# Kernel tuning notes

Measured on AMD Instinct MI355X. Metric: run time of the kernel, lower is better.

The kernel has to match this reference:

```python
import jax, jax.numpy as jnp
import numpy as np

H = 256      # hidden_units
NB = 2       # num_blocks
NH = 4       # num_heads
E = 8        # num_experts
K = 2        # top_k
L = 200      # maxlen
B = 128      # batch
ITEM = 100000
USER = 50000


def _ln(x, w, b, eps):
    m = x.mean(-1, keepdims=True)
    v = ((x - m) ** 2).mean(-1, keepdims=True)
    return (x - m) / jnp.sqrt(v + eps) * w + b


def setup_inputs() -> dict:
    key = jax.random.key(0)
    ks = iter(jax.random.split(key, 48))

    def n(shape, s=0.02):
        return jax.random.normal(next(ks), shape, jnp.float32) * s

    item_emb = n((ITEM + 1, H)).at[0].set(0.0)   # padding_idx=0
    pos_emb = n((L + 1, H)).at[0].set(0.0)
    user_emb = n((USER + 1, H)).at[0].set(0.0)
    return dict(
        user_ids=jax.random.randint(next(ks), (B,), 1, USER + 1),
        log_seqs=jax.random.randint(next(ks), (B, L), 0, ITEM + 1),
        item_ids=jax.random.randint(next(ks), (B,), 1, ITEM + 1),
        item_emb=item_emb, pos_emb=pos_emb, user_emb=user_emb,
        ln1_w=jnp.ones((NB, H)), ln1_b=jnp.zeros((NB, H)),
        inproj_w=n((NB, 3 * H, H)), inproj_b=jnp.zeros((NB, 3 * H)),
        outproj_w=n((NB, H, H)), outproj_b=jnp.zeros((NB, H)),
        ln2_w=jnp.ones((NB, H)), ln2_b=jnp.zeros((NB, H)),
        gate_w=n((NB, E, H)), gate_b=jnp.zeros((NB, E)),
        e_w1=n((NB, E, H, H)), e_b1=jnp.zeros((NB, E, H)),
        e_w2=n((NB, E, H, H)), e_b2=jnp.zeros((NB, E, H)),
        moeln_w=jnp.ones((NB, H)), moeln_b=jnp.zeros((NB, H)),
        lastln_w=jnp.ones((H,)), lastln_b=jnp.zeros((H,)),
    )


def reference(user_ids, log_seqs, item_ids, item_emb, pos_emb, user_emb,
              ln1_w, ln1_b, inproj_w, inproj_b, outproj_w, outproj_b,
              ln2_w, ln2_b, gate_w, gate_b, e_w1, e_b1, e_w2, e_b2,
              moeln_w, moeln_b, lastln_w, lastln_b):
    hd = H // NH
    # embeddings (padding id 0 -> zero rows)
    x = item_emb[log_seqs] * jnp.sqrt(jnp.float32(H))          # [B,L,H]
    poss = jnp.arange(1, L + 1)[None, :] * (log_seqs != 0)      # 0 where padded
    x = x + pos_emb[poss]
    causal = jnp.tril(jnp.ones((L, L), bool))

    for i in range(NB):
        # pre-LN query, raw x as key/value (matches original)
        q_in = _ln(x, ln1_w[i], ln1_b[i], 1e-8)
        wq, wk, wv = jnp.split(inproj_w[i], 3, axis=0)
        bq, bk, bv = jnp.split(inproj_b[i], 3)
        q = (q_in @ wq.T + bq).reshape(B, L, NH, hd)
        k = (x @ wk.T + bk).reshape(B, L, NH, hd)
        v = (x @ wv.T + bv).reshape(B, L, NH, hd)
        s = jnp.einsum('bqnd,bknd->bnqk', q, k) / jnp.sqrt(jnp.float32(hd))
        s = jnp.where(causal, s, -jnp.inf)
        a = jax.nn.softmax(s, axis=-1)
        ctx = jnp.einsum('bnqk,bknd->bqnd', a, v).reshape(B, L, H)
        mha = ctx @ outproj_w[i].T + outproj_b[i]
        x = q_in + mha
        x = _ln(x, ln2_w[i], ln2_b[i], 1e-8)

        # SparseMoE: top-k gate, all-expert dense compute, masked combine
        gl = jnp.einsum('bsh,eh->bse', x, gate_w[i]) + gate_b[i]
        w, idx = jax.lax.top_k(gl, K)
        w = jax.nn.softmax(w, axis=-1)
        comb = (jax.nn.one_hot(idx, E) * w[..., None]).sum(-2)   # [B,L,E]
        h = jax.nn.relu(jnp.einsum('bsh,ehd->besd', x, e_w1[i])
                        + e_b1[i][None, :, None, :])              # [B,E,L,H]
        y = jnp.einsum('besd,edh->besh', h, e_w2[i]) + e_b2[i][None, :, None, :]
        moe = jnp.einsum('bse,besh->bsh', comb, y)
        x = _ln(x + moe, moeln_w[i], moeln_b[i], 1e-5)

    x = _ln(x, lastln_w, lastln_b, 1e-8)
    final = x[:, -1, :] + user_emb[user_ids]
    return (final * item_emb[item_ids]).sum(-1)   # [B] logits
```

## Files before the change

kernel.cpp:

```cpp
#include <hip/hip_runtime.h>
#include <math.h>

#define H 256
#define NHEAD 4
#define HD 64
#define NEXP 8
#define SEQL 200
#define BATCH 128
#define NF (BATCH*SEQL)
#define KT 64
#define QT 64
#define QW 8

__device__ __forceinline__ float blk_sum256(float v, float* s4) {
    #pragma unroll
    for (int o = 32; o > 0; o >>= 1) v += __shfl_xor(v, o, 64);
    __syncthreads();
    if ((threadIdx.x & 63) == 0) s4[threadIdx.x >> 6] = v;
    __syncthreads();
    return s4[0] + s4[1] + s4[2] + s4[3];
}

__global__ __launch_bounds__(256) void embed_ln_kernel(
    const int* __restrict__ seqs, const float* __restrict__ item_emb,
    const float* __restrict__ pos_emb, float* __restrict__ x,
    float* __restrict__ xln, const float* __restrict__ w, const float* __restrict__ b)
{
    __shared__ float s4[4];
    int n = blockIdx.x, t = threadIdx.x;
    int id = seqs[n];
    int pos = (id != 0) ? (n % SEQL) + 1 : 0;
    float v = item_emb[(size_t)id*H + t] * 16.0f + pos_emb[(size_t)pos*H + t];
    x[(size_t)n*H + t] = v;
    float mean = blk_sum256(v, s4) * (1.f/H);
    float d = v - mean;
    float var = blk_sum256(d*d, s4) * (1.f/H);
    xln[(size_t)n*H + t] = d * rsqrtf(var + 1e-8f) * w[t] + b[t];
}

__global__ __launch_bounds__(256) void ln_kernel(
    const float* __restrict__ in, const float* __restrict__ res,
    float* __restrict__ out, const float* __restrict__ w, const float* __restrict__ b,
    float eps, int base, int step)
{
    __shared__ float s4[4];
    int r = blockIdx.x, t = threadIdx.x;
    float v = in[(size_t)(base + r*step)*H + t];
    if (res) v += res[(size_t)r*H + t];
    float mean = blk_sum256(v, s4) * (1.f/H);
    float d = v - mean;
    float var = blk_sum256(d*d, s4) * (1.f/H);
    out[(size_t)r*H + t] = d * rsqrtf(var + eps) * w[t] + b[t];
}

__global__ __launch_bounds__(256) void ln2_gate_kernel(
    const float* __restrict__ in, const float* __restrict__ res,
    float* __restrict__ out, const float* __restrict__ w, const float* __restrict__ b,
    const float* __restrict__ gw, const float* __restrict__ gb,
    int* __restrict__ top_idx, float* __restrict__ top_w)
{
    __shared__ float s4[4];
    __shared__ float xs[H];
    __shared__ float gl[NEXP];
    int n = blockIdx.x, t = threadIdx.x;
    float v = in[(size_t)n*H + t] + res[(size_t)n*H + t];
    float mean = blk_sum256(v, s4) * (1.f/H);
    float d = v - mean;
    float var = blk_sum256(d*d, s4) * (1.f/H);
    float r = d * rsqrtf(var + 1e-8f) * w[t] + b[t];
    out[(size_t)n*H + t] = r;
    xs[t] = r;
    __syncthreads();
    int wv = t >> 6, lane = t & 63;
    float xv[4];
    #pragma unroll
    for (int c = 0; c < 4; ++c) xv[c] = xs[lane + (c<<6)];
    #pragma unroll
    for (int s = 0; s < 2; ++s) {
        int e = wv*2 + s;
        float acc = 0.f;
        #pragma unroll
        for (int c = 0; c < 4; ++c) acc += xv[c] * gw[(size_t)e*H + lane + (c<<6)];
        #pragma unroll
        for (int o = 32; o > 0; o >>= 1) acc += __shfl_xor(acc, o, 64);
        if (lane == 0) gl[e] = acc + gb[e];
    }
    __syncthreads();
    if (t == 0) {
        int i0 = 0;
        for (int e = 1; e < NEXP; ++e) if (gl[e] > gl[i0]) i0 = e;
        int i1 = -1;
        for (int e = 0; e < NEXP; ++e) { if (e == i0) continue; if (i1 < 0 || gl[e] > gl[i1]) i1 = e; }
        float e1 = expf(gl[i1] - gl[i0]);
        float w0 = 1.f / (1.f + e1);
        top_idx[n*2+0] = i0; top_idx[n*2+1] = i1;
        top_w[n*2+0] = w0;  top_w[n*2+1] = 1.f - w0;
    }
}

__global__ __launch_bounds__(256) void moe_ln_kernel(
    const float* __restrict__ x, const float* __restrict__ ybuf,
    const int* __restrict__ tok_pair, const float* __restrict__ top_w,
    float* __restrict__ out, const float* __restrict__ w, const float* __restrict__ b,
    float eps)
{
    __shared__ float s4[4];
    int r = blockIdx.x, t = threadIdx.x;
    int p0 = tok_pair[r*2], p1 = tok_pair[r*2+1];
    float v = x[(size_t)r*H + t]
            + top_w[r*2+0] * ybuf[(size_t)p0*H + t]
            + top_w[r*2+1] * ybuf[(size_t)p1*H + t];
    float mean = blk_sum256(v, s4) * (1.f/H);
    float d = v - mean;
    float var = blk_sum256(d*d, s4) * (1.f/H);
    out[(size_t)r*H + t] = d * rsqrtf(var + eps) * w[t] + b[t];
}

__global__ __launch_bounds__(256) void gemm_nt(
    const float* __restrict__ A, const float* __restrict__ W,
    const float* __restrict__ bias, float* __restrict__ out, int nrows)
{
    __shared__ float As[16][68];
    __shared__ float Ws[16][68];
    int r0 = blockIdx.x * 64;
    if (r0 >= nrows) return;
    int c0 = blockIdx.y * 64;
    int tid = threadIdx.x;
    int tx = tid & 15, ty = tid >> 4;
    int lrow = tid >> 2, lkg = (tid & 3) << 2;
    float acc[4][4] = {};
    for (int kk = 0; kk < H; kk += 16) {
        float4 av = make_float4(0.f,0.f,0.f,0.f);
        int gr = r0 + lrow;
        if (gr < nrows) av = *(const float4*)(A + (size_t)gr*H + kk + lkg);
        As[lkg+0][lrow]=av.x; As[lkg+1][lrow]=av.y; As[lkg+2][lrow]=av.z; As[lkg+3][lrow]=av.w;
        float4 wv = *(const float4*)(W + (size_t)(c0+lrow)*H + kk + lkg);
        Ws[lkg+0][lrow]=wv.x; Ws[lkg+1][lrow]=wv.y; Ws[lkg+2][lrow]=wv.z; Ws[lkg+3][lrow]=wv.w;
        __syncthreads();
        #pragma unroll
        for (int k = 0; k < 16; ++k) {
            float4 a = *(const float4*)&As[k][ty<<2];
            float4 bv = *(const float4*)&Ws[k][tx<<2];
            float aa[4] = {a.x,a.y,a.z,a.w};
            float bb[4] = {bv.x,bv.y,bv.z,bv.w};
            #pragma unroll
            for (int ii = 0; ii < 4; ++ii)
                #pragma unroll
                for (int jj = 0; jj < 4; ++jj)
                    acc[ii][jj] += aa[ii] * bb[jj];
        }
        __syncthreads();
    }
    #pragma unroll
    for (int ii = 0; ii < 4; ++ii) {
        int gr = r0 + (ty<<2) + ii;
        if (gr < nrows) {
            #pragma unroll
            for (int jj = 0; jj < 4; ++jj) {
                int gc = c0 + (tx<<2) + jj;
                out[(size_t)gr*H + gc] = acc[ii][jj] + bias[gc];
            }
        }
    }
}

template<int GATHER, int RELU, int BT>
__device__ __forceinline__ void gemm128_body(
    const float* __restrict__ A, const float* __restrict__ W,
    const float* __restrict__ bias, float* __restrict__ out, int nrows,
    const int* __restrict__ pair_tok)
{
    __shared__ float As[2][16*132];
    __shared__ float Ws[2][16*132];
    int r0 = blockIdx.x * 128;
    if (r0 >= nrows) return;
    int c0 = blockIdx.y * 128;
    int tid = threadIdx.x;
    int tx = tid & 15, ty = tid >> 4;
    int lrow = tid >> 1, lkg = (tid & 1) << 3;
    int ar = r0 + lrow;
    bool va = ar < nrows;
    int ga = ar;
    if (GATHER) ga = va ? pair_tok[r0 + lrow] : 0;
    const float* ap = A + (size_t)(va ? ga : 0)*H + lkg;
    const float* wpT = W + (size_t)(c0 + lrow)*H + lkg;
    int kr0 = tid >> 5, cg = (tid & 31) << 2;
    const float* wpN0 = W + (size_t)kr0*H + c0 + cg;
    const float* wpN1 = wpN0 + (size_t)8*H;
    const float4 f4z = make_float4(0.f,0.f,0.f,0.f);
    float4 av0, av1, wv0, wv1;

#define G128_LOAD(S) {                                                        \
        int kk_ = (S)*16;                                                     \
        if (va) { av0 = *(const float4*)(ap + kk_);                           \
                  av1 = *(const float4*)(ap + kk_ + 4); }                     \
        else { av0 = f4z; av1 = f4z; }                                        \
        if (BT) { wv0 = *(const float4*)(wpT + kk_);                          \
                  wv1 = *(const float4*)(wpT + kk_ + 4); }                    \
        else { wv0 = *(const float4*)(wpN0 + (size_t)kk_*H);                  \
               wv1 = *(const float4*)(wpN1 + (size_t)kk_*H); } }

#define G128_WRITE(BI) {                                                      \
        float* as_ = As[BI]; float* ws_ = Ws[BI];                             \
        as_[(lkg+0)*132 + lrow]=av0.x; as_[(lkg+1)*132 + lrow]=av0.y;         \
        as_[(lkg+2)*132 + lrow]=av0.z; as_[(lkg+3)*132 + lrow]=av0.w;         \
        as_[(lkg+4)*132 + lrow]=av1.x; as_[(lkg+5)*132 + lrow]=av1.y;         \
        as_[(lkg+6)*132 + lrow]=av1.z; as_[(lkg+7)*132 + lrow]=av1.w;         \
        if (BT) {                                                             \
            ws_[(lkg+0)*132 + lrow]=wv0.x; ws_[(lkg+1)*132 + lrow]=wv0.y;     \
            ws_[(lkg+2)*132 + lrow]=wv0.z; ws_[(lkg+3)*132 + lrow]=wv0.w;     \
            ws_[(lkg+4)*132 + lrow]=wv1.x; ws_[(lkg+5)*132 + lrow]=wv1.y;     \
            ws_[(lkg+6)*132 + lrow]=wv1.z; ws_[(lkg+7)*132 + lrow]=wv1.w;     \
        } else {                                                              \
            *(float4*)&ws_[kr0*132 + cg]     = wv0;                           \
            *(float4*)&ws_[(kr0+8)*132 + cg] = wv1;                           \
        } }

    const int NS = H/16;
    float acc[8][8] = {};
    G128_LOAD(0)
    G128_WRITE(0)
    G128_LOAD(1)
    __syncthreads();
    for (int s = 0; s < NS; ++s) {
        int cur = s & 1;
        if (s + 1 < NS) {
            G128_WRITE((s+1) & 1)
            if (s + 2 < NS) G128_LOAD(s+2)
        }
        const float* as = As[cur];
        const float* bs = Ws[cur];
        #pragma unroll
        for (int k = 0; k < 16; ++k) {
            float4 a0 = *(const float4*)&as[k*132 + (ty<<2)];
            float4 a1 = *(const float4*)&as[k*132 + 64 + (ty<<2)];
            float4 b0 = *(const float4*)&bs[k*132 + (tx<<2)];
            float4 b1 = *(const float4*)&bs[k*132 + 64 + (tx<<2)];
            float aa[8] = {a0.x,a0.y,a0.z,a0.w,a1.x,a1.y,a1.z,a1.w};
            float bb[8] = {b0.x,b0.y,b0.z,b0.w,b1.x,b1.y,b1.z,b1.w};
            #pragma unroll
            for (int ii = 0; ii < 8; ++ii)
                #pragma unroll
                for (int jj = 0; jj < 8; ++jj)
                    acc[ii][jj] += aa[ii] * bb[jj];
        }
        __syncthreads();
    }
#undef G128_LOAD
#undef G128_WRITE
    #pragma unroll
    for (int hr = 0; hr < 2; ++hr)
        #pragma unroll
        for (int ii = 0; ii < 4; ++ii) {
            int row = r0 + 64*hr + (ty<<2) + ii;
            if (row < nrows) {
                #pragma unroll
                for (int hc = 0; hc < 2; ++hc) {
                    int col = c0 + 64*hc + (tx<<2);
                    #pragma unroll
                    for (int jj = 0; jj < 4; ++jj) {
                        float o = acc[4*hr+ii][4*hc+jj] + bias[col+jj];
                        if (RELU) o = fmaxf(o, 0.f);
                        out[(size_t)row*H + col + jj] = o;
                    }
                }
            }
        }
}

__global__ __launch_bounds__(256) void gemm_nt128z(
    const float* __restrict__ A0, const float* __restrict__ A1,
    const float* __restrict__ Wbase, const float* __restrict__ biasbase,
    float* __restrict__ outbase, int nrows)
{
    int z = blockIdx.z;
    const float* A = (z == 0) ? A0 : A1;
    gemm128_body<0,0,1>(A, Wbase + (size_t)z*H*H, biasbase + (size_t)z*H,
                        outbase + (size_t)z*NF*H, nrows, nullptr);
}

__global__ __launch_bounds__(256) void gemm_nt128(
    const float* __restrict__ A, const float* __restrict__ W,
    const float* __restrict__ bias, float* __restrict__ out, int nrows)
{
    gemm128_body<0,0,1>(A, W, bias, out, nrows, nullptr);
}

__global__ __launch_bounds__(256) void moe1_128(
    const float* __restrict__ X, const float* __restrict__ W1base,
    const float* __restrict__ b1base, const int* __restrict__ pair_tok,
    const int* __restrict__ offsets, const int* __restrict__ counts,
    float* __restrict__ hbuf)
{
    int e = blockIdx.z;
    int cnt = counts[e], off = offsets[e];
    gemm128_body<1,1,0>(X, W1base + (size_t)e*H*H, b1base + (size_t)e*H,
                        hbuf + (size_t)off*H, cnt, pair_tok + off);
}

__global__ __launch_bounds__(256) void moe2_128(
    const float* __restrict__ Hbuf, const float* __restrict__ W2base,
    const float* __restrict__ b2base, const int* __restrict__ offsets,
    const int* __restrict__ counts, float* __restrict__ ybuf)
{
    int e = blockIdx.z;
    int cnt = counts[e], off = offsets[e];
    gemm128_body<0,0,0>(Hbuf + (size_t)off*H, W2base + (size_t)e*H*H, b2base + (size_t)e*H,
                        ybuf + (size_t)off*H, cnt, nullptr);
}

__global__ __launch_bounds__(512) void attn_kernel(
    const float* __restrict__ qbuf, const float* __restrict__ kbuf,
    const float* __restrict__ vbuf, float* __restrict__ ctx, int nq, int nz)
{
    __shared__ float kv[KT*(HD+4)];
    __shared__ float qs[QT][HD+4];
    __shared__ float ps[QT][KT+4];
    int bx = blockIdx.x;
    int b = bx / nz, z = bx % nz;
    int h = blockIdx.y;
    int qbase = z * QT;
    int nqt = nq - qbase;
    if (nqt <= 0) return;
    if (nqt > QT) nqt = QT;
    int tid = threadIdx.x, w = tid >> 6, lane = tid & 63;
    int off = SEQL - nq;
    for (int i = tid; i < QT*(HD/4); i += 512) {
        int row = i >> 4, c4 = (i & 15) << 2;
        float4 qv = make_float4(0.f,0.f,0.f,0.f);
        if (row < nqt) qv = *(const float4*)(qbuf + (size_t)(b*nq + qbase + row)*H + h*HD + c4);
        *(float4*)&qs[row][c4] = qv;
    }
    float m[QW], l[QW], acc[QW];
    #pragma unroll
    for (int i = 0; i < QW; ++i) { m[i] = -3e30f; l[i] = 0.f; acc[i] = 0.f; }
    int wq0 = w * QW;
    int wqn = nqt - wq0; if (wqn > QW) wqn = QW;
    int wmaxpos = qbase + wq0 + (wqn > 0 ? wqn - 1 : 0) + off;
    int ntiles = (qbase + nqt - 1 + off) / KT + 1;
    int q_sub = lane >> 3, kq = lane & 7;
    for (int t = 0; t < ntiles; ++t) {
        int kbase = t * KT;
        bool active = (wqn > 0) && (kbase <= wmaxpos);
        __syncthreads();
        for (int i = tid; i < KT*(HD/4); i += 512) {
            int row = i >> 4, c4 = (i & 15) << 2;
            int key = kbase + row;
            float4 kvv = make_float4(0.f,0.f,0.f,0.f);
            if (key < SEQL) kvv = *(const float4*)(kbuf + (size_t)(b*SEQL + key)*H + h*HD + c4);
            *(float4*)&kv[row*(HD+4) + c4] = kvv;
        }
        __syncthreads();
        if (active) {
            float s[QW];
            #pragma unroll
            for (int qi = 0; qi < QW; ++qi) s[qi] = 0.f;
            #pragma unroll 4
            for (int d4 = 0; d4 < HD; d4 += 4) {
                float4 k4 = *(const float4*)&kv[lane*(HD+4) + d4];
                #pragma unroll
                for (int qi = 0; qi < QW; ++qi) {
                    float4 q4 = *(const float4*)&qs[wq0+qi][d4];
                    s[qi] += k4.x*q4.x + k4.y*q4.y + k4.z*q4.z + k4.w*q4.w;
                }
            }
            #pragma unroll
            for (int qi = 0; qi < QW; ++qi) {
                if (qi < wqn) {
                    int qpos = qbase + wq0 + qi + off;
                    bool valid = (kbase + lane) <= qpos;
                    ps[wq0+qi][lane] = valid ? s[qi]*0.125f : -3e30f;
                }
            }
        }
        __syncthreads();
        {
            int key = kbase + lane;
            bool kval = key < SEQL;
            const float* vp = vbuf + (size_t)(b*SEQL + (kval ? key : 0))*H + h*HD;
            #pragma unroll
            for (int it = 0; it < 2; ++it) {
                int c4 = ((it << 3) + w) << 2;
                float4 vv = make_float4(0.f,0.f,0.f,0.f);
                if (kval) vv = *(const float4*)(vp + c4);
                kv[(c4+0)*(KT+4) + lane] = vv.x;
                kv[(c4+1)*(KT+4) + lane] = vv.y;
                kv[(c4+2)*(KT+4) + lane] = vv.z;
                kv[(c4+3)*(KT+4) + lane] = vv.w;
            }
        }
        __syncthreads();
        if (active) {
            float mq = m[0];
            #pragma unroll
            for (int i = 1; i < QW; ++i) if (q_sub == i) mq = m[i];
            const float2* pr = (const float2*)&ps[wq0+q_sub][kq*8];
            float2 a0 = pr[0], a1 = pr[1], a2 = pr[2], a3 = pr[3];
            float mloc = fmaxf(fmaxf(fmaxf(a0.x,a0.y), fmaxf(a1.x,a1.y)),
                               fmaxf(fmaxf(a2.x,a2.y), fmaxf(a3.x,a3.y)));
            float tm = mloc;
            #pragma unroll
            for (int o = 1; o < 8; o <<= 1) tm = fmaxf(tm, __shfl_xor(tm, o, 64));
            float mn = fmaxf(mq, tm);
            float p0 = expf(a0.x-mn), p1 = expf(a0.y-mn), p2 = expf(a1.x-mn), p3 = expf(a1.y-mn);
            float p4 = expf(a2.x-mn), p5 = expf(a2.y-mn), p6 = expf(a3.x-mn), p7 = expf(a3.y-mn);
            float psum = ((p0+p1)+(p2+p3)) + ((p4+p5)+(p6+p7));
            #pragma unroll
            for (int o = 1; o < 8; o <<= 1) psum += __shfl_xor(psum, o, 64);
            float2* pw = (float2*)&ps[wq0+q_sub][kq*8];
            pw[0] = make_float2(p0,p1); pw[1] = make_float2(p2,p3);
            pw[2] = make_float2(p4,p5); pw[3] = make_float2(p6,p7);
            #pragma unroll
            for (int qi = 0; qi < QW; ++qi) {
                float tmv = __shfl(tm, qi*8, 64);
                float psv = __shfl(psum, qi*8, 64);
                if (qi < wqn) {
                    float mn2 = fmaxf(m[qi], tmv);
                    float scl = expf(m[qi] - mn2);
                    l[qi] = l[qi]*scl + psv;
                    acc[qi] *= scl;
                    m[qi] = mn2;
                }
            }
            #pragma unroll 4
            for (int k4 = 0; k4 < KT; k4 += 4) {
                float4 v4 = *(const float4*)&kv[lane*(KT+4) + k4];
                #pragma unroll
                for (int qi = 0; qi < QW; ++qi) {
                    if (qi < wqn) {
                        float4 p4v = *(const float4*)&ps[wq0+qi][k4];
                        acc[qi] += p4v.x*v4.x + p4v.y*v4.y + p4v.z*v4.z + p4v.w*v4.w;
                    }
                }
            }
        }
    }
    #pragma unroll
    for (int qi = 0; qi < QW; ++qi) {
        if (qi < wqn) {
            ctx[(size_t)(b*nq + qbase + wq0 + qi)*H + h*HD + lane] = acc[qi] / l[qi];
        }
    }
}

__global__ __launch_bounds__(256) void count_kernel(
    const int* __restrict__ top_idx, int* __restrict__ counts, int nrows)
{
    __shared__ int hist[NEXP];
    int tid = threadIdx.x;
    if (tid < NEXP) hist[tid] = 0;
    __syncthreads();
    int n = blockIdx.x * 256 + tid;
    if (n < nrows) {
        atomicAdd(&hist[top_idx[n*2+0]], 1);
        atomicAdd(&hist[top_idx[n*2+1]], 1);
    }
    __syncthreads();
    if (tid < NEXP && hist[tid] > 0) atomicAdd(&counts[tid], hist[tid]);
}

__global__ void scan_kernel(const int* __restrict__ counts, int* __restrict__ offsets,
                            int* __restrict__ cursor)
{
    int s = 0;
    for (int e = 0; e < NEXP; ++e) { offsets[e] = s; cursor[e] = s; s += counts[e]; }
}

__global__ __launch_bounds__(256) void scatter_kernel(
    const int* __restrict__ top_idx,
    int* __restrict__ cursor, int* __restrict__ pair_tok, int* __restrict__ tok_pair, int nrows)
{
    __shared__ int lcnt[NEXP];
    __shared__ int lbase[NEXP];
    int tid = threadIdx.x;
    if (tid < NEXP) lcnt[tid] = 0;
    __syncthreads();
    int n = blockIdx.x * 256 + tid;
    int e0 = 0, e1 = 0, p0 = 0, p1 = 0;
    bool act = n < nrows;
    if (act) {
        e0 = top_idx[n*2+0]; e1 = top_idx[n*2+1];
        p0 = atomicAdd(&lcnt[e0], 1);
        p1 = atomicAdd(&lcnt[e1], 1);
    }
    __syncthreads();
    if (tid < NEXP) lbase[tid] = (lcnt[tid] > 0) ? atomicAdd(&cursor[tid], lcnt[tid]) : 0;
    __syncthreads();
    if (act) {
        int q0 = lbase[e0] + p0, q1 = lbase[e1] + p1;
        pair_tok[q0] = n; pair_tok[q1] = n;
        tok_pair[n*2+0] = q0; tok_pair[n*2+1] = q1;
    }
}

__global__ __launch_bounds__(256) void moe_gemm1(
    const float* __restrict__ X, const float* __restrict__ W1base,
    const float* __restrict__ b1base, const int* __restrict__ pair_tok,
    const int* __restrict__ offsets, const int* __restrict__ counts,
    float* __restrict__ hbuf)
{
    int e = blockIdx.z;
    int cnt = counts[e];
    int r0 = blockIdx.x * 64;
    if (r0 >= cnt) return;
    int off = offsets[e];
    int c0 = blockIdx.y * 64;
    const float* W = W1base + (size_t)e * H * H;
    const float* bias = b1base + (size_t)e * H;
    __shared__ float As[16][68];
    __shared__ float Bs[16][68];
    int tid = threadIdx.x, tx = tid & 15, ty = tid >> 4;
    int lrow = tid >> 2, lkg = (tid & 3) << 2;
    float acc[4][4] = {};
    for (int kk = 0; kk < H; kk += 16) {
        float4 av = make_float4(0.f,0.f,0.f,0.f);
        int pr = r0 + lrow;
        if (pr < cnt) {
            int tok = pair_tok[off + pr];
            av = *(const float4*)(X + (size_t)tok*H + kk + lkg);
        }
        As[lkg+0][lrow]=av.x; As[lkg+1][lrow]=av.y; As[lkg+2][lrow]=av.z; As[lkg+3][lrow]=av.w;
        float4 wv = *(const float4*)(W + (size_t)(kk+ty)*H + c0 + (tx<<2));
        *(float4*)&Bs[ty][tx<<2] = wv;
        __syncthreads();
        #pragma unroll
        for (int k = 0; k < 16; ++k) {
            float4 a = *(const float4*)&As[k][ty<<2];
            float4 bv = *(const float4*)&Bs[k][tx<<2];
            float aa[4] = {a.x,a.y,a.z,a.w};
            float bb[4] = {bv.x,bv.y,bv.z,bv.w};
            #pragma unroll
            for (int ii = 0; ii < 4; ++ii)
                #pragma unroll
                for (int jj = 0; jj < 4; ++jj)
                    acc[ii][jj] += aa[ii] * bb[jj];
        }
        __syncthreads();
    }
    #pragma unroll
    for (int ii = 0; ii < 4; ++ii) {
        int pr = r0 + (ty<<2) + ii;
        if (pr < cnt) {
            #pragma unroll
            for (int jj = 0; jj < 4; ++jj) {
                int gc = c0 + (tx<<2) + jj;
                hbuf[(size_t)(off+pr)*H + gc] = fmaxf(acc[ii][jj] + bias[gc], 0.f);
            }
        }
    }
}

__global__ __launch_bounds__(256) void moe_gemm2(
    const float* __restrict__ Hbuf, const float* __restrict__ W2base,
    const float* __restrict__ b2base, const int* __restrict__ offsets,
    const int* __restrict__ counts, float* __restrict__ ybuf)
{
    int e = blockIdx.z;
    int cnt = counts[e];
    int r0 = blockIdx.x * 64;
    if (r0 >= cnt) return;
    int off = offsets[e];
    int c0 = blockIdx.y * 64;
    const float* W = W2base + (size_t)e * H * H;
    const float* bias = b2base + (size_t)e * H;
    __shared__ float As[16][68];
    __shared__ float Bs[16][68];
    int tid = threadIdx.x, tx = tid & 15, ty = tid >> 4;
    int lrow = tid >> 2, lkg = (tid & 3) << 2;
    float acc[4][4] = {};
    for (int kk = 0; kk < H; kk += 16) {
        float4 av = make_float4(0.f,0.f,0.f,0.f);
        int pr = r0 + lrow;
        if (pr < cnt) av = *(const float4*)(Hbuf + (size_t)(off+pr)*H + kk + lkg);
        As[lkg+0][lrow]=av.x; As[lkg+1][lrow]=av.y; As[lkg+2][lrow]=av.z; As[lkg+3][lrow]=av.w;
        float4 wv = *(const float4*)(W + (size_t)(kk+ty)*H + c0 + (tx<<2));
        *(float4*)&Bs[ty][tx<<2] = wv;
        __syncthreads();
        #pragma unroll
        for (int k = 0; k < 16; ++k) {
            float4 a = *(const float4*)&As[k][ty<<2];
            float4 bv = *(const float4*)&Bs[k][tx<<2];
            float aa[4] = {a.x,a.y,a.z,a.w};
            float bb[4] = {bv.x,bv.y,bv.z,bv.w};
            #pragma unroll
            for (int ii = 0; ii < 4; ++ii)
                #pragma unroll
                for (int jj = 0; jj < 4; ++jj)
                    acc[ii][jj] += aa[ii] * bb[jj];
        }
        __syncthreads();
    }
    #pragma unroll
    for (int ii = 0; ii < 4; ++ii) {
        int pr = r0 + (ty<<2) + ii;
        if (pr < cnt) {
            #pragma unroll
            for (int jj = 0; jj < 4; ++jj) {
                int gc = c0 + (tx<<2) + jj;
                ybuf[(size_t)(off+pr)*H + gc] = acc[ii][jj] + bias[gc];
            }
        }
    }
}

__global__ void zero_kernel(float* __restrict__ p, int n) {
    int i = blockIdx.x * 256 + threadIdx.x;
    if (i < n) p[i] = 0.f;
}

__global__ __launch_bounds__(256) void final_kernel(
    const float* __restrict__ xf, const float* __restrict__ lnw, const float* __restrict__ lnb,
    const float* __restrict__ user_emb, const float* __restrict__ item_emb,
    const int* __restrict__ user_ids, const int* __restrict__ item_ids, float* __restrict__ out)
{
    __shared__ float s4[4];
    int bb = blockIdx.x, t = threadIdx.x;
    float v = xf[(size_t)bb*H + t];
    float mean = blk_sum256(v, s4) * (1.f/H);
    float d = v - mean;
    float var = blk_sum256(d*d, s4) * (1.f/H);
    float lnv = d * rsqrtf(var + 1e-8f) * lnw[t] + lnb[t];
    float fin = lnv + user_emb[(size_t)user_ids[bb]*H + t];
    float prod = fin * item_emb[(size_t)item_ids[bb]*H + t];
    float tot = blk_sum256(prod, s4);
    if (t == 0) out[bb] = tot;
}

extern "C" void kernel_launch(void* const* d_in, const int* in_sizes, int n_in,
                              void* d_out, int out_size, void* d_ws, size_t ws_size,
                              hipStream_t stream)
{
    (void)in_sizes; (void)n_in; (void)out_size; (void)ws_size;
    const int*   user_ids  = (const int*)d_in[0];
    const int*   log_seqs  = (const int*)d_in[1];
    const int*   item_ids  = (const int*)d_in[2];
    const float* item_emb  = (const float*)d_in[3];
    const float* pos_emb   = (const float*)d_in[4];
    const float* user_emb  = (const float*)d_in[5];
    const float* ln1_w     = (const float*)d_in[6];
    const float* ln1_b     = (const float*)d_in[7];
    const float* inproj_w  = (const float*)d_in[8];
    const float* inproj_b  = (const float*)d_in[9];
    const float* outproj_w = (const float*)d_in[10];
    const float* outproj_b = (const float*)d_in[11];
    const float* ln2_w     = (const float*)d_in[12];
    const float* ln2_b     = (const float*)d_in[13];
    const float* gate_w    = (const float*)d_in[14];
    const float* gate_b    = (const float*)d_in[15];
    const float* e_w1      = (const float*)d_in[16];
    const float* e_b1      = (const float*)d_in[17];
    const float* e_w2      = (const float*)d_in[18];
    const float* e_b2      = (const float*)d_in[19];
    const float* moeln_w   = (const float*)d_in[20];
    const float* moeln_b   = (const float*)d_in[21];
    const float* lastln_w  = (const float*)d_in[22];
    const float* lastln_b  = (const float*)d_in[23];

    float* ws = (float*)d_ws;
    const size_t NFH = (size_t)NF * H;
    float* buf0 = ws;
    float* buf1 = buf0 + NFH;
    float* buf2 = buf1 + NFH;
    float* buf3 = buf2 + NFH;
    float* buf4 = buf3 + NFH;
    float* s0   = buf4 + NFH;
    float* s1   = s0 + (size_t)BATCH*H;
    float* s2   = s1 + (size_t)BATCH*H;
    float* s3   = s2 + (size_t)BATCH*H;
    float* s6   = s3 + (size_t)BATCH*H;
    float* s4   = s6 + (size_t)BATCH*H;
    float* s5   = s4 + (size_t)2*BATCH*H;
    float* top_w   = s5 + (size_t)2*BATCH*H;
    int*   top_idx = (int*)(top_w + (size_t)NF*2);
    int*   pair_tok= top_idx + (size_t)NF*2;
    int*   tok_pair= pair_tok + (size_t)NF*2;
    int*   counts  = tok_pair + (size_t)NF*2;
    int*   offsets = counts + NEXP;
    int*   cursor  = offsets + NEXP;

    dim3 blk(256);
    dim3 ablk(512);
    dim3 g128((NF+127)/128, H/128);
    dim3 g128z3((NF+127)/128, H/128, 3);
    dim3 g128z2((NF+127)/128, H/128, 2);
    dim3 gsmall((BATCH+63)/64, H/64);
    dim3 m128((NF+127)/128, H/128, NEXP);
    dim3 msmall((BATCH+63)/64, H/64, NEXP);

    {
        const int i = 0;
        const float* Wq = inproj_w + (size_t)i*3*H*H;
        const float* bq = inproj_b + (size_t)i*3*H;
        embed_ln_kernel<<<NF, blk, 0, stream>>>(log_seqs, item_emb, pos_emb, buf0, buf1,
                                                ln1_w + i*H, ln1_b + i*H);
        gemm_nt128z<<<g128z3, blk, 0, stream>>>(buf1, buf0, Wq, bq, buf2, NF);
        attn_kernel<<<dim3(BATCH*4, NHEAD), ablk, 0, stream>>>(buf2, buf3, buf4, buf2, SEQL, 4);
        gemm_nt128<<<g128, blk, 0, stream>>>(buf2, outproj_w + (size_t)i*H*H, outproj_b + i*H, buf3, NF);
        ln2_gate_kernel<<<NF, blk, 0, stream>>>(buf1, buf3, buf0, ln2_w + i*H, ln2_b + i*H,
                                                gate_w + (size_t)i*NEXP*H, gate_b + i*NEXP,
                                                top_idx, top_w);
        zero_kernel<<<1, 32, 0, stream>>>((float*)counts, NEXP);
        count_kernel<<<(NF+255)/256, blk, 0, stream>>>(top_idx, counts, NF);
        scan_kernel<<<1, 1, 0, stream>>>(counts, offsets, cursor);
        scatter_kernel<<<(NF+255)/256, blk, 0, stream>>>(top_idx, cursor, pair_tok, tok_pair, NF);
        moe1_128<<<m128, blk, 0, stream>>>(buf0, e_w1 + (size_t)i*NEXP*H*H, e_b1 + (size_t)i*NEXP*H,
                                           pair_tok, offsets, counts, buf3);
        moe2_128<<<m128, blk, 0, stream>>>(buf3, e_w2 + (size_t)i*NEXP*H*H, e_b2 + (size_t)i*NEXP*H,
                                           offsets, counts, buf1);
        moe_ln_kernel<<<NF, blk, 0, stream>>>(buf0, buf1, tok_pair, top_w, buf3,
                                              moeln_w + i*H, moeln_b + i*H, 1e-5f);
    }

    {
        const int i = 1;
        const float* Wq = inproj_w + (size_t)i*3*H*H;
        const float* bq = inproj_b + (size_t)i*3*H;
        float* X = buf3;
        ln_kernel<<<BATCH, blk, 0, stream>>>(X, nullptr, s0, ln1_w + i*H, ln1_b + i*H, 1e-8f, SEQL-1, SEQL);
        gemm_nt<<<gsmall, blk, 0, stream>>>(s0, Wq, bq, s1, BATCH);
        gemm_nt128z<<<g128z2, blk, 0, stream>>>(X, X, Wq + (size_t)H*H, bq + H, buf0, NF);
        attn_kernel<<<dim3(BATCH, NHEAD), ablk, 0, stream>>>(s1, buf0, buf1, s2, 1, 1);
        gemm_nt<<<gsmall, blk, 0, stream>>>(s2, outproj_w + (size_t)i*H*H, outproj_b + i*H, s3, BATCH);
        ln2_gate_kernel<<<BATCH, blk, 0, stream>>>(s0, s3, s2, ln2_w + i*H, ln2_b + i*H,
                                                   gate_w + (size_t)i*NEXP*H, gate_b + i*NEXP,
                                                   top_idx, top_w);
        zero_kernel<<<1, 32, 0, stream>>>((float*)counts, NEXP);
        count_kernel<<<1, blk, 0, stream>>>(top_idx, counts, BATCH);
        scan_kernel<<<1, 1, 0, stream>>>(counts, offsets, cursor);
        scatter_kernel<<<1, blk, 0, stream>>>(top_idx, cursor, pair_tok, tok_pair, BATCH);
        moe_gemm1<<<msmall, blk, 0, stream>>>(s2, e_w1 + (size_t)i*NEXP*H*H, e_b1 + (size_t)i*NEXP*H,
                                              pair_tok, offsets, counts, s4);
        moe_gemm2<<<msmall, blk, 0, stream>>>(s4, e_w2 + (size_t)i*NEXP*H*H, e_b2 + (size_t)i*NEXP*H,
                                              offsets, counts, s5);
        moe_ln_kernel<<<BATCH, blk, 0, stream>>>(s2, s5, tok_pair, top_w, s6,
                                                 moeln_w + i*H, moeln_b + i*H, 1e-5f);
    }

    final_kernel<<<BATCH, blk, 0, stream>>>(s6, lastln_w, lastln_b, user_emb, item_emb,
                                            user_ids, item_ids, (float*)d_out);
}
```

Measured before the change: 945.6 us.

## Replace FP32 SIMT GEMMs with split-bf16 MFMA GEMMs using pre-split weights

The large dense and MoE expert GEMMs change from FP32 register-tiled FMA loops to bf16 MFMA 16x16x32 instructions. Each operand is split into high and low bf16 parts and combined with three MFMAs, which keeps close to FP32 accuracy. Weights are split, and for the experts transposed, into bf16 hi/lo buffers by new kernels at the start of every call. Activations are split on the fly from global memory with no LDS staging, so A tiles are re-read once per column block. The attention grid is also reindexed to use blockIdx.z for query tiles.

```diff
diff --git a/kernel.cpp b/kernel.cpp
--- a/kernel.cpp
+++ b/kernel.cpp
@@ -12,6 +12,31 @@
 #define QT 64
 #define QW 8
 
+typedef __bf16 bf16x8 __attribute__((ext_vector_type(8)));
+typedef float  f32x4  __attribute__((ext_vector_type(4)));
+
+__device__ __forceinline__ void split8(const float* __restrict__ p, bf16x8& hi, bf16x8& lo, bool valid) {
+    if (valid) {
+        float4 a = *(const float4*)p;
+        float4 b = *(const float4*)(p + 4);
+        float x[8] = {a.x,a.y,a.z,a.w,b.x,b.y,b.z,b.w};
+        #pragma unroll
+        for (int j = 0; j < 8; ++j) {
+            __bf16 h = (__bf16)x[j];
+            hi[j] = h;
+            lo[j] = (__bf16)(x[j] - (float)h);
+        }
+    } else {
+        #pragma unroll
+        for (int j = 0; j < 8; ++j) { hi[j] = (__bf16)0.f; lo[j] = (__bf16)0.f; }
+    }
+}
+
+#define MFMA3(AH,AL,BH,BL,ACC) \
+    ACC = __builtin_amdgcn_mfma_f32_16x16x32_bf16(AH, BH, ACC, 0, 0, 0); \
+    ACC = __builtin_amdgcn_mfma_f32_16x16x32_bf16(AH, BL, ACC, 0, 0, 0); \
+    ACC = __builtin_amdgcn_mfma_f32_16x16x32_bf16(AL, BH, ACC, 0, 0, 0);
+
 __device__ __forceinline__ float blk_sum256(float v, float* s4) {
     #pragma unroll
     for (int o = 32; o > 0; o >>= 1) v += __shfl_xor(v, o, 64);
@@ -19,6 +44,31 @@
     if ((threadIdx.x & 63) == 0) s4[threadIdx.x >> 6] = v;
     __syncthreads();
     return s4[0] + s4[1] + s4[2] + s4[3];
+}
+
+__global__ __launch_bounds__(256) void split_plain(
+    const float* __restrict__ in, __bf16* __restrict__ hi, __bf16* __restrict__ lo, int n)
+{
+    for (int i = blockIdx.x * 256 + threadIdx.x; i < n; i += gridDim.x * 256) {
+        float x = in[i];
+        __bf16 h = (__bf16)x;
+        hi[i] = h;
+        lo[i] = (__bf16)(x - (float)h);
+    }
+}
+
+__global__ __launch_bounds__(256) void split_trans(
+    const float* __restrict__ in, __bf16* __restrict__ hi, __bf16* __restrict__ lo, int nmats)
+{
+    int n = nmats * H * H;
+    for (int i = blockIdx.x * 256 + threadIdx.x; i < n; i += gridDim.x * 256) {
+        int m = i / (H*H), rem = i % (H*H);
+        int nn = rem / H, k = rem % H;
+        float x = in[(size_t)m*H*H + (size_t)k*H + nn];
+        __bf16 h = (__bf16)x;
+        hi[i] = h;
+        lo[i] = (__bf16)(x - (float)h);
+    }
 }
 
 __global__ __launch_bounds__(256) void embed_ln_kernel(
@@ -164,161 +214,101 @@
     }
 }
 
-template<int GATHER, int RELU, int BT>
-__device__ __forceinline__ void gemm128_body(
-    const float* __restrict__ A, const float* __restrict__ W,
+template<int GATHER, int RELU>
+__device__ __forceinline__ void mfma64_body(
+    const float* __restrict__ A, const __bf16* __restrict__ Whi, const __bf16* __restrict__ Wlo,
     const float* __restrict__ bias, float* __restrict__ out, int nrows,
     const int* __restrict__ pair_tok)
 {
-    __shared__ float As[2][16*132];
-    __shared__ float Ws[2][16*132];
-    int r0 = blockIdx.x * 128;
+    int r0 = blockIdx.x * 64;
     if (r0 >= nrows) return;
-    int c0 = blockIdx.y * 128;
+    int c0 = blockIdx.y * 64;
     int tid = threadIdx.x;
-    int tx = tid & 15, ty = tid >> 4;
-    int lrow = tid >> 1, lkg = (tid & 1) << 3;
-    int ar = r0 + lrow;
-    bool va = ar < nrows;
-    int ga = ar;
-    if (GATHER) ga = va ? pair_tok[r0 + lrow] : 0;
-    const float* ap = A + (size_t)(va ? ga : 0)*H + lkg;
-    const float* wpT = W + (size_t)(c0 + lrow)*H + lkg;
-    int kr0 = tid >> 5, cg = (tid & 31) << 2;
-    const float* wpN0 = W + (size_t)kr0*H + c0 + cg;
-    const float* wpN1 = wpN0 + (size_t)8*H;
-    const float4 f4z = make_float4(0.f,0.f,0.f,0.f);
-    float4 av0, av1, wv0, wv1;
-
-#define G128_LOAD(S) {                                                        \
-        int kk_ = (S)*16;                                                     \
-        if (va) { av0 = *(const float4*)(ap + kk_);                           \
-                  av1 = *(const float4*)(ap + kk_ + 4); }                     \
-        else { av0 = f4z; av1 = f4z; }                                        \
-        if (BT) { wv0 = *(const float4*)(wpT + kk_);                          \
-                  wv1 = *(const float4*)(wpT + kk_ + 4); }                    \
-        else { wv0 = *(const float4*)(wpN0 + (size_t)kk_*H);                  \
-               wv1 = *(const float4*)(wpN1 + (size_t)kk_*H); } }
-
-#define G128_WRITE(BI) {                                                      \
-        float* as_ = As[BI]; float* ws_ = Ws[BI];                             \
-        as_[(lkg+0)*132 + lrow]=av0.x; as_[(lkg+1)*132 + lrow]=av0.y;         \
-        as_[(lkg+2)*132 + lrow]=av0.z; as_[(lkg+3)*132 + lrow]=av0.w;         \
-        as_[(lkg+4)*132 + lrow]=av1.x; as_[(lkg+5)*132 + lrow]=av1.y;         \
-        as_[(lkg+6)*132 + lrow]=av1.z; as_[(lkg+7)*132 + lrow]=av1.w;         \
-        if (BT) {                                                             \
-            ws_[(lkg+0)*132 + lrow]=wv0.x; ws_[(lkg+1)*132 + lrow]=wv0.y;     \
-            ws_[(lkg+2)*132 + lrow]=wv0.z; ws_[(lkg+3)*132 + lrow]=wv0.w;     \
-            ws_[(lkg+4)*132 + lrow]=wv1.x; ws_[(lkg+5)*132 + lrow]=wv1.y;     \
-            ws_[(lkg+6)*132 + lrow]=wv1.z; ws_[(lkg+7)*132 + lrow]=wv1.w;     \
-        } else {                                                              \
-            *(float4*)&ws_[kr0*132 + cg]     = wv0;                           \
-            *(float4*)&ws_[(kr0+8)*132 + cg] = wv1;                           \
-        } }
-
-    const int NS = H/16;
-    float acc[8][8] = {};
-    G128_LOAD(0)
-    G128_WRITE(0)
-    G128_LOAD(1)
-    __syncthreads();
-    for (int s = 0; s < NS; ++s) {
-        int cur = s & 1;
-        if (s + 1 < NS) {
-            G128_WRITE((s+1) & 1)
-            if (s + 2 < NS) G128_LOAD(s+2)
-        }
-        const float* as = As[cur];
-        const float* bs = Ws[cur];
+    int wid = tid >> 6, lane = tid & 63;
+    int wm = wid >> 1, wn = wid & 1;
+    int rbase = r0 + wm*32, cbase = c0 + wn*32;
+    int lr = lane & 15, lk = (lane >> 4) << 3;
+    f32x4 acc[2][2] = {};
+    int ar0 = rbase + lr, ar1 = ar0 + 16;
+    bool v0 = ar0 < nrows, v1 = ar1 < nrows;
+    int ga0 = ar0, ga1 = ar1;
+    if (GATHER) { ga0 = v0 ? pair_tok[ar0] : 0; ga1 = v1 ? pair_tok[ar1] : 0; }
+    const float* ap0 = A + (size_t)(v0 ? ga0 : 0)*H + lk;
+    const float* ap1 = A + (size_t)(v1 ? ga1 : 0)*H + lk;
+    size_t woff = (size_t)(cbase + lr)*H + lk;
+    #pragma unroll
+    for (int kk = 0; kk < H; kk += 32) {
+        bf16x8 ah0, al0, ah1, al1;
+        split8(ap0 + kk, ah0, al0, v0);
+        split8(ap1 + kk, ah1, al1, v1);
+        bf16x8 bh0 = *(const bf16x8*)(Whi + woff + kk);
+        bf16x8 bl0 = *(const bf16x8*)(Wlo + woff + kk);
+        bf16x8 bh1 = *(const bf16x8*)(Whi + woff + (size_t)16*H + kk);
+        bf16x8 bl1 = *(const bf16x8*)(Wlo + woff + (size_t)16*H + kk);
+        MFMA3(ah0, al0, bh0, bl0, acc[0][0]);
+        MFMA3(ah0, al0, bh1, bl1, acc[0][1]);
+        MFMA3(ah1, al1, bh0, bl0, acc[1][0]);
+        MFMA3(ah1, al1, bh1, bl1, acc[1][1]);
+    }
+    int lro = (lane >> 4) << 2;
+    #pragma unroll
+    for (int mi = 0; mi < 2; ++mi)
         #pragma unroll
-        for (int k = 0; k < 16; ++k) {
-            float4 a0 = *(const float4*)&as[k*132 + (ty<<2)];
-            float4 a1 = *(const float4*)&as[k*132 + 64 + (ty<<2)];
-            float4 b0 = *(const float4*)&bs[k*132 + (tx<<2)];
-            float4 b1 = *(const float4*)&bs[k*132 + 64 + (tx<<2)];
-            float aa[8] = {a0.x,a0.y,a0.z,a0.w,a1.x,a1.y,a1.z,a1.w};
-            float bb[8] = {b0.x,b0.y,b0.z,b0.w,b1.x,b1.y,b1.z,b1.w};
-            #pragma unroll
-            for (int ii = 0; ii < 8; ++ii)
-                #pragma unroll
-                for (int jj = 0; jj < 8; ++jj)
-                    acc[ii][jj] += aa[ii] * bb[jj];
-        }
-        __syncthreads();
-    }
-#undef G128_LOAD
-#undef G128_WRITE
-    #pragma unroll
-    for (int hr = 0; hr < 2; ++hr)
-        #pragma unroll
-        for (int ii = 0; ii < 4; ++ii) {
-            int row = r0 + 64*hr + (ty<<2) + ii;
-            if (row < nrows) {
-                #pragma unroll
-                for (int hc = 0; hc < 2; ++hc) {
-                    int col = c0 + 64*hc + (tx<<2);
-                    #pragma unroll
-                    for (int jj = 0; jj < 4; ++jj) {
-                        float o = acc[4*hr+ii][4*hc+jj] + bias[col+jj];
-                        if (RELU) o = fmaxf(o, 0.f);
-                        out[(size_t)row*H + col + jj] = o;
-                    }
+        for (int ni = 0; ni < 2; ++ni)
+            #pragma unroll
+            for (int j = 0; j < 4; ++j) {
+                int row = rbase + mi*16 + lro + j;
+                int col = cbase + ni*16 + lr;
+                if (row < nrows) {
+                    float o = acc[mi][ni][j] + bias[col];
+                    if (RELU) o = fmaxf(o, 0.f);
+                    out[(size_t)row*H + col] = o;
                 }
             }
-        }
-}
-
-__global__ __launch_bounds__(256) void gemm_nt128z(
+}
+
+__global__ __launch_bounds__(256) void mfma_z(
     const float* __restrict__ A0, const float* __restrict__ A1,
-    const float* __restrict__ Wbase, const float* __restrict__ biasbase,
-    float* __restrict__ outbase, int nrows)
+    const __bf16* __restrict__ Whi, const __bf16* __restrict__ Wlo,
+    const float* __restrict__ biasbase, float* __restrict__ outbase, int nrows)
 {
     int z = blockIdx.z;
     const float* A = (z == 0) ? A0 : A1;
-    gemm128_body<0,0,1>(A, Wbase + (size_t)z*H*H, biasbase + (size_t)z*H,
-                        outbase + (size_t)z*NF*H, nrows, nullptr);
-}
-
-__global__ __launch_bounds__(256) void gemm_nt128(
-    const float* __restrict__ A, const float* __restrict__ W,
-    const float* __restrict__ bias, float* __restrict__ out, int nrows)
-{
-    gemm128_body<0,0,1>(A, W, bias, out, nrows, nullptr);
-}
-
-__global__ __launch_bounds__(256) void moe1_128(
-    const float* __restrict__ X, const float* __restrict__ W1base,
+    mfma64_body<0,0>(A, Whi + (size_t)z*H*H, Wlo + (size_t)z*H*H,
+                     biasbase + (size_t)z*H, outbase + (size_t)z*NF*H, nrows, nullptr);
+}
+
+__global__ __launch_bounds__(256) void mfma_moe1(
+    const float* __restrict__ X, const __bf16* __restrict__ Whi, const __bf16* __restrict__ Wlo,
     const float* __restrict__ b1base, const int* __restrict__ pair_tok,
     const int* __restrict__ offsets, const int* __restrict__ counts,
     float* __restrict__ hbuf)
 {
     int e = blockIdx.z;
     int cnt = counts[e], off = offsets[e];
-    gemm128_body<1,1,0>(X, W1base + (size_t)e*H*H, b1base + (size_t)e*H,
-                        hbuf + (size_t)off*H, cnt, pair_tok + off);
-}
-
-__global__ __launch_bounds__(256) void moe2_128(
-    const float* __restrict__ Hbuf, const float* __restrict__ W2base,
+    mfma64_body<1,1>(X, Whi + (size_t)e*H*H, Wlo + (size_t)e*H*H,
+                     b1base + (size_t)e*H, hbuf + (size_t)off*H, cnt, pair_tok + off);
+}
+
+__global__ __launch_bounds__(256) void mfma_moe2(
+    const float* __restrict__ Hbuf, const __bf16* __restrict__ Whi, const __bf16* __restrict__ Wlo,
     const float* __restrict__ b2base, const int* __restrict__ offsets,
     const int* __restrict__ counts, float* __restrict__ ybuf)
 {
     int e = blockIdx.z;
     int cnt = counts[e], off = offsets[e];
-    gemm128_body<0,0,0>(Hbuf + (size_t)off*H, W2base + (size_t)e*H*H, b2base + (size_t)e*H,
-                        ybuf + (size_t)off*H, cnt, nullptr);
+    mfma64_body<0,0>(Hbuf + (size_t)off*H, Whi + (size_t)e*H*H, Wlo + (size_t)e*H*H,
+                     b2base + (size_t)e*H, ybuf + (size_t)off*H, cnt, nullptr);
 }
 
 __global__ __launch_bounds__(512) void attn_kernel(
     const float* __restrict__ qbuf, const float* __restrict__ kbuf,
-    const float* __restrict__ vbuf, float* __restrict__ ctx, int nq, int nz)
+    const float* __restrict__ vbuf, float* __restrict__ ctx, int nq)
 {
     __shared__ float kv[KT*(HD+4)];
     __shared__ float qs[QT][HD+4];
     __shared__ float ps[QT][KT+4];
-    int bx = blockIdx.x;
-    int b = bx / nz, z = bx % nz;
-    int h = blockIdx.y;
+    int b = blockIdx.x, h = blockIdx.y, z = blockIdx.z;
     int qbase = z * QT;
     int nqt = nq - qbase;
     if (nqt <= 0) return;
@@ -677,25 +667,40 @@
     int*   counts  = tok_pair + (size_t)NF*2;
     int*   offsets = counts + NEXP;
     int*   cursor  = offsets + NEXP;
+    const size_t W_IP = (size_t)2*3*H*H;
+    const size_t W_OP = (size_t)2*H*H;
+    const size_t W_E  = (size_t)2*NEXP*H*H;
+    __bf16* ip_hi = (__bf16*)(cursor + 64);
+    __bf16* ip_lo = ip_hi + W_IP;
+    __bf16* op_hi = ip_lo + W_IP;
+    __bf16* op_lo = op_hi + W_OP;
+    __bf16* e1_hi = op_lo + W_OP;
+    __bf16* e1_lo = e1_hi + W_E;
+    __bf16* e2_hi = e1_lo + W_E;
+    __bf16* e2_lo = e2_hi + W_E;
 
     dim3 blk(256);
     dim3 ablk(512);
-    dim3 g128((NF+127)/128, H/128);
-    dim3 g128z3((NF+127)/128, H/128, 3);
-    dim3 g128z2((NF+127)/128, H/128, 2);
+    dim3 m64z3(NF/64, H/64, 3);
+    dim3 m64z2(NF/64, H/64, 2);
+    dim3 m64z1(NF/64, H/64, 1);
+    dim3 m64e(NF/64, H/64, NEXP);
     dim3 gsmall((BATCH+63)/64, H/64);
-    dim3 m128((NF+127)/128, H/128, NEXP);
     dim3 msmall((BATCH+63)/64, H/64, NEXP);
+
+    split_plain<<<512, blk, 0, stream>>>(inproj_w,  ip_hi, ip_lo, (int)W_IP);
+    split_plain<<<256, blk, 0, stream>>>(outproj_w, op_hi, op_lo, (int)W_OP);
+    split_trans<<<1024, blk, 0, stream>>>(e_w1, e1_hi, e1_lo, 2*NEXP);
+    split_trans<<<1024, blk, 0, stream>>>(e_w2, e2_hi, e2_lo, 2*NEXP);
 
     {
         const int i = 0;
-        const float* Wq = inproj_w + (size_t)i*3*H*H;
         const float* bq = inproj_b + (size_t)i*3*H;
         embed_ln_kernel<<<NF, blk, 0, stream>>>(log_seqs, item_emb, pos_emb, buf0, buf1,
                                                 ln1_w + i*H, ln1_b + i*H);
-        gemm_nt128z<<<g128z3, blk, 0, stream>>>(buf1, buf0, Wq, bq, buf2, NF);
-        attn_kernel<<<dim3(BATCH*4, NHEAD), ablk, 0, stream>>>(buf2, buf3, buf4, buf2, SEQL, 4);
-        gemm_nt128<<<g128, blk, 0, stream>>>(buf2, outproj_w + (size_t)i*H*H, outproj_b + i*H, buf3, NF);
+        mfma_z<<<m64z3, blk, 0, stream>>>(buf1, buf0, ip_hi, ip_lo, bq, buf2, NF);
+        attn_kernel<<<dim3(BATCH, NHEAD, (SEQL+QT-1)/QT), ablk, 0, stream>>>(buf2, buf3, buf4, buf2, SEQL);
+        mfma_z<<<m64z1, blk, 0, stream>>>(buf2, buf2, op_hi, op_lo, outproj_b, buf3, NF);
         ln2_gate_kernel<<<NF, blk, 0, stream>>>(buf1, buf3, buf0, ln2_w + i*H, ln2_b + i*H,
                                                 gate_w + (size_t)i*NEXP*H, gate_b + i*NEXP,
                                                 top_idx, top_w);
@@ -703,10 +708,10 @@
         count_kernel<<<(NF+255)/256, blk, 0, stream>>>(top_idx, counts, NF);
         scan_kernel<<<1, 1, 0, stream>>>(counts, offsets, cursor);
         scatter_kernel<<<(NF+255)/256, blk, 0, stream>>>(top_idx, cursor, pair_tok, tok_pair, NF);
-        moe1_128<<<m128, blk, 0, stream>>>(buf0, e_w1 + (size_t)i*NEXP*H*H, e_b1 + (size_t)i*NEXP*H,
-                                           pair_tok, offsets, counts, buf3);
-        moe2_128<<<m128, blk, 0, stream>>>(buf3, e_w2 + (size_t)i*NEXP*H*H, e_b2 + (size_t)i*NEXP*H,
-                                           offsets, counts, buf1);
+        mfma_moe1<<<m64e, blk, 0, stream>>>(buf0, e1_hi, e1_lo, e_b1 + (size_t)i*NEXP*H,
+                                            pair_tok, offsets, counts, buf3);
+        mfma_moe2<<<m64e, blk, 0, stream>>>(buf3, e2_hi, e2_lo, e_b2 + (size_t)i*NEXP*H,
+                                            offsets, counts, buf1);
         moe_ln_kernel<<<NF, blk, 0, stream>>>(buf0, buf1, tok_pair, top_w, buf3,
                                               moeln_w + i*H, moeln_b + i*H, 1e-5f);
     }
@@ -718,8 +723,9 @@
         float* X = buf3;
         ln_kernel<<<BATCH, blk, 0, stream>>>(X, nullptr, s0, ln1_w + i*H, ln1_b + i*H, 1e-8f, SEQL-1, SEQL);
         gemm_nt<<<gsmall, blk, 0, stream>>>(s0, Wq, bq, s1, BATCH);
-        gemm_nt128z<<<g128z2, blk, 0, stream>>>(X, X, Wq + (size_t)H*H, bq + H, buf0, NF);
-        attn_kernel<<<dim3(BATCH, NHEAD), ablk, 0, stream>>>(s1, buf0, buf1, s2, 1, 1);
+        mfma_z<<<m64z2, blk, 0, stream>>>(X, X, ip_hi + (size_t)3*H*H + (size_t)H*H,
+                                          ip_lo + (size_t)3*H*H + (size_t)H*H, bq + H, buf0, NF);
+        attn_kernel<<<dim3(BATCH, NHEAD, 1), ablk, 0, stream>>>(s1, buf0, buf1, s2, 1);
         gemm_nt<<<gsmall, blk, 0, stream>>>(s2, outproj_w + (size_t)i*H*H, outproj_b + i*H, s3, BATCH);
         ln2_gate_kernel<<<BATCH, blk, 0, stream>>>(s0, s3, s2, ln2_w + i*H, ln2_b + i*H,
                                                    gate_w + (size_t)i*NEXP*H, gate_b + i*NEXP,
```

Measured after the change: 916.9 us. 3.0% less time.
